# Kernel optimization log

Hardware: AMD Instinct MI355X
Metric: run time of the kernel (lower is better)

Reference implementation:

```python
import jax, jax.numpy as jnp
import numpy as np

D = 1024
W_SIZE = 512
K_ENGRAMS = 16
REPEAT = W_SIZE // K_ENGRAMS  # 32
LN_EPS = 1e-5


def setup_inputs() -> dict:
    key = jax.random.key(0)
    ks = jax.random.split(key, 6)
    B, NW = 4, 16
    engrams = jax.random.normal(ks[0], (B, NW, K_ENGRAMS, D), dtype=jnp.float32)
    pos_emb = 0.02 * jax.random.normal(ks[1], (1, 1, W_SIZE, D), dtype=jnp.float32)
    w1 = 0.02 * jax.random.normal(ks[2], (D, D), dtype=jnp.float32)
    b1 = jnp.zeros((D,), dtype=jnp.float32)
    w2 = 0.02 * jax.random.normal(ks[3], (D, D), dtype=jnp.float32)
    b2 = jnp.zeros((D,), dtype=jnp.float32)
    gamma = jnp.ones((D,), dtype=jnp.float32)
    beta = jnp.zeros((D,), dtype=jnp.float32)
    return {"engrams": engrams, "pos_emb": pos_emb, "w1": w1, "b1": b1,
            "w2": w2, "b2": b2, "gamma": gamma, "beta": beta}


def reference(engrams, pos_emb, w1, b1, w2, b2, gamma, beta):
    # (B, nw, K, d) -> (B, nw, W, d) via repeat_interleave along axis 2
    x = jnp.repeat(engrams, REPEAT, axis=2) + pos_emb
    # refine MLP: Linear -> GELU (exact) -> Linear, with residual
    h = jax.nn.gelu(jnp.einsum('bnwd,de->bnwe', x, w1.T) + b1, approximate=False)
    x = x + jnp.einsum('bnwd,de->bnwe', h, w2.T) + b2
    # LayerNorm over last dim
    mu = jnp.mean(x, axis=-1, keepdims=True)
    var = jnp.mean(jnp.square(x - mu), axis=-1, keepdims=True)
    return (x - mu) * jax.lax.rsqrt(var + LN_EPS) * gamma + beta
```

## Files before the change

### kernel.cpp

```cpp
#include <hip/hip_runtime.h>
#include <hip/hip_bf16.h>
#include <math.h>

#define D_DIM 1024
#define NROWS 32768
#define NE_ROWS 1024
#define A1_ROWS 1536
#define NT2 16

typedef __attribute__((ext_vector_type(8))) short bf16x8;
typedef __attribute__((ext_vector_type(4))) float f32x4;

static __device__ __forceinline__ ushort f2bf(float f) {
  union { float f; unsigned u; } un; un.f = f;
  unsigned u = un.u;
  unsigned r = u + 0x7fffu + ((u >> 16) & 1u);
  return (ushort)(r >> 16);
}
static __device__ __forceinline__ float bf2f(ushort h) {
  union { unsigned u; float f; } un; un.u = ((unsigned)h) << 16;
  return un.f;
}
static __device__ __forceinline__ float gelu_exact(float v) {
  return 0.5f * v * (1.0f + erff(v * 0.70710678118654752f));
}

__global__ void cast_all_kernel(const float* __restrict__ w1, const float* __restrict__ w2,
                                const float* __restrict__ eng, const float* __restrict__ pos,
                                ushort* __restrict__ dst) {
  int i = blockIdx.x * blockDim.x + threadIdx.x;
  float4 v;
  if (i < 262144) v = ((const float4*)w1)[i];
  else if (i < 524288) v = ((const float4*)w2)[i - 262144];
  else if (i < 786432) v = ((const float4*)eng)[i - 524288];
  else v = ((const float4*)pos)[i - 786432];
  ushort4 o;
  o.x = f2bf(v.x); o.y = f2bf(v.y); o.z = f2bf(v.z); o.w = f2bf(v.w);
  ((ushort4*)dst)[i] = o;
}

__global__ __launch_bounds__(256) void gemm_bt(const ushort* __restrict__ A,
                                               const ushort* __restrict__ B,
                                               float* __restrict__ C,
                                               int M, int N, int K) {
  __shared__ ushort sA[128 * 64];
  __shared__ ushort sB[128 * 64];

  int nwg = gridDim.x;
  int bid = blockIdx.x;
  if ((nwg & 7) == 0) {
    int cpx = nwg >> 3;
    bid = (bid & 7) * cpx + (bid >> 3);
  }
  int ntn = N >> 7;
  int mt = bid / ntn, nt = bid % ntn;
  int brow = mt << 7, bcol = nt << 7;

  int tid = threadIdx.x;
  int wv = tid >> 6, lane = tid & 63;
  int wm = (wv >> 1) << 6, wn = (wv & 1) << 6;
  int lr = lane & 15, lk = lane >> 4;
  int srow = lane >> 3;
  int scolsw = (((lane & 7) ^ ((lane >> 3) & 7)) << 3);

  f32x4 acc[4][4];
#pragma unroll
  for (int m = 0; m < 4; ++m)
#pragma unroll
    for (int n = 0; n < 4; ++n) acc[m][n] = (f32x4){0.f, 0.f, 0.f, 0.f};

  for (int k0 = 0; k0 < K; k0 += 64) {
    __syncthreads();
#pragma unroll
    for (int j = 0; j < 4; ++j) {
      int c = (wv << 2) + j;
      int row = (c << 3) + srow;
      const ushort* gA = A + (brow + row) * K + k0 + scolsw;
      const ushort* gB = B + (bcol + row) * K + k0 + scolsw;
      __builtin_amdgcn_global_load_lds(
          (const __attribute__((address_space(1))) unsigned int*)gA,
          (__attribute__((address_space(3))) unsigned int*)&sA[c << 9], 16, 0, 0);
      __builtin_amdgcn_global_load_lds(
          (const __attribute__((address_space(1))) unsigned int*)gB,
          (__attribute__((address_space(3))) unsigned int*)&sB[c << 9], 16, 0, 0);
    }
    __syncthreads();
#pragma unroll
    for (int kk = 0; kk < 2; ++kk) {
      int rdoff = (((kk << 2) | lk) ^ (lr & 7)) << 3;
      bf16x8 af[4], bfr[4];
#pragma unroll
      for (int m = 0; m < 4; ++m)
        af[m] = *(const bf16x8*)&sA[(wm + (m << 4) + lr) * 64 + rdoff];
#pragma unroll
      for (int n = 0; n < 4; ++n)
        bfr[n] = *(const bf16x8*)&sB[(wn + (n << 4) + lr) * 64 + rdoff];
#pragma unroll
      for (int m = 0; m < 4; ++m)
#pragma unroll
        for (int n = 0; n < 4; ++n)
          acc[m][n] = __builtin_amdgcn_mfma_f32_16x16x32_bf16(af[m], bfr[n], acc[m][n], 0, 0, 0);
    }
  }

#pragma unroll
  for (int m = 0; m < 4; ++m)
#pragma unroll
    for (int n = 0; n < 4; ++n)
#pragma unroll
      for (int i = 0; i < 4; ++i) {
        int row = brow + wm + (m << 4) + (lk << 2) + i;
        int col = bcol + wn + (n << 4) + lr;
        C[(long)row * N + col] = acc[m][n][i];
      }
}

__global__ __launch_bounds__(256) void gelu_kernel(const float* __restrict__ xw1,
                                                   const float* __restrict__ b1,
                                                   ushort* __restrict__ h) {
  int r = blockIdx.x;
  int t = threadIdx.x;
  int bn = r >> 9;
  int w = r & 511;
  int er = bn * 16 + (w >> 5);
  float4 e = ((const float4*)(xw1 + er * D_DIM))[t];
  float4 p = ((const float4*)(xw1 + (NE_ROWS + w) * D_DIM))[t];
  float4 b = ((const float4*)b1)[t];
  ushort4 o;
  o.x = f2bf(gelu_exact(e.x + p.x + b.x));
  o.y = f2bf(gelu_exact(e.y + p.y + b.y));
  o.z = f2bf(gelu_exact(e.z + p.z + b.z));
  o.w = f2bf(gelu_exact(e.w + p.w + b.w));
  ((ushort4*)(h + (long)r * D_DIM))[t] = o;
}

__global__ __launch_bounds__(512, 2) void gemm2_8ph(const ushort* __restrict__ A,
                                                    const ushort* __restrict__ B,
                                                    ushort* __restrict__ Y) {
  __shared__ ushort sA[2][2][8192];
  __shared__ ushort sB[2][2][8192];
  const int K = 1024;

  int bid = blockIdx.x;
  bid = (bid & 7) * 64 + (bid >> 3);
  int mt = bid >> 2, nt = bid & 3;
  long brow = (long)mt << 8;
  int bcol = nt << 8;

  int tid = threadIdx.x;
  int wv = tid >> 6, l = tid & 63;
  int wr = wv >> 2, wc = wv & 3;
  int lr = l & 15, lk = l >> 4;

  int sr = (wv << 4) + (l >> 2);
  int slog = ((l & 3) ^ ((l >> 3) & 3)) << 3;
  const ushort* aS = A + (brow + sr) * (long)K + slog;
  const ushort* bS = B + (size_t)(bcol + sr) * K + slog;

  int rdswz = (lk ^ ((lr >> 1) & 3)) << 3;
  int aO = (((wr << 7) + lr) << 5) + rdswz;
  int bO = (((wc << 6) + lr) << 5) + rdswz;

  f32x4 acc[8][4];
#pragma unroll
  for (int m = 0; m < 8; ++m)
#pragma unroll
    for (int n = 0; n < 4; ++n) acc[m][n] = (f32x4){0.f, 0.f, 0.f, 0.f};

#define STG(SS, SRC, kt, kkh) do {                                                   \
    int p_ = (kt) & 1; int o_ = ((kt) << 6) + ((kkh) << 5);                          \
    __builtin_amdgcn_global_load_lds(                                                \
      (const __attribute__((address_space(1))) unsigned int*)((SRC) + o_),           \
      (__attribute__((address_space(3))) unsigned int*)&SS[p_][kkh][wv << 9], 16, 0, 0); \
    __builtin_amdgcn_global_load_lds(                                                \
      (const __attribute__((address_space(1))) unsigned int*)((SRC) + o_ + 131072),  \
      (__attribute__((address_space(3))) unsigned int*)&SS[p_][kkh][(wv << 9) + 4096], 16, 0, 0); \
  } while (0)

#define BAR asm volatile("s_barrier" ::: "memory")
#define MFMA16(MOFS, BF)                                                             \
    __builtin_amdgcn_s_setprio(1);                                                   \
    _Pragma("unroll")                                                                \
    for (int m = 0; m < 4; ++m)                                                      \
      _Pragma("unroll")                                                              \
      for (int n = 0; n < 4; ++n)                                                    \
        acc[m + MOFS][n] = __builtin_amdgcn_mfma_f32_16x16x32_bf16(af[m], BF[n], acc[m + MOFS][n], 0, 0, 0); \
    __builtin_amdgcn_s_setprio(0)

  STG(sA, aS, 0, 0); STG(sB, bS, 0, 0); STG(sA, aS, 0, 1); STG(sB, bS, 0, 1);
  asm volatile("s_waitcnt vmcnt(0)" ::: "memory");
  BAR;

  for (int t = 0; t < NT2; ++t) {
    int p = t & 1;
    bf16x8 af[4], bf[4];
#pragma unroll
    for (int n = 0; n < 4; ++n) bf[n] = *(const bf16x8*)&sB[p][0][bO + (n << 9)];
#pragma unroll
    for (int m = 0; m < 4; ++m) af[m] = *(const bf16x8*)&sA[p][0][aO + (m << 9)];
    if (t + 1 < NT2) STG(sA, aS, t + 1, 0);
    BAR;
    MFMA16(0, bf);
    BAR;
#pragma unroll
    for (int m = 0; m < 4; ++m) af[m] = *(const bf16x8*)&sA[p][0][aO + ((m + 4) << 9)];
    if (t + 1 < NT2) STG(sB, bS, t + 1, 0);
    BAR;
    MFMA16(4, bf);
    if (t == NT2 - 1) asm volatile("s_waitcnt vmcnt(0)" ::: "memory");
    else              asm volatile("s_waitcnt vmcnt(4)" ::: "memory");
    BAR;
#pragma unroll
    for (int n = 0; n < 4; ++n) bf[n] = *(const bf16x8*)&sB[p][1][bO + (n << 9)];
#pragma unroll
    for (int m = 0; m < 4; ++m) af[m] = *(const bf16x8*)&sA[p][1][aO + (m << 9)];
    if (t + 1 < NT2) STG(sA, aS, t + 1, 1);
    BAR;
    MFMA16(0, bf);
    BAR;
#pragma unroll
    for (int m = 0; m < 4; ++m) af[m] = *(const bf16x8*)&sA[p][1][aO + ((m + 4) << 9)];
    if (t + 1 < NT2) STG(sB, bS, t + 1, 1);
    BAR;
    MFMA16(4, bf);
    if (t < NT2 - 1) asm volatile("s_waitcnt vmcnt(4)" ::: "memory");
    BAR;
  }
#undef STG
#undef BAR
#undef MFMA16

#pragma unroll
  for (int m = 0; m < 8; ++m)
#pragma unroll
    for (int n = 0; n < 4; ++n) {
      int col = bcol + (wc << 6) + (n << 4) + lr;
#pragma unroll
      for (int i = 0; i < 4; ++i) {
        long row = brow + (wr << 7) + (m << 4) + (lk << 2) + i;
        Y[(row << 11) + col] = f2bf(acc[m][n][i]);
      }
    }
}

__global__ __launch_bounds__(256) void ln_kernel(const float* __restrict__ eng,
                                                 const float* __restrict__ pos,
                                                 const float* __restrict__ b2,
                                                 const float* __restrict__ gamma,
                                                 const float* __restrict__ beta,
                                                 float* __restrict__ out) {
  __shared__ float red[8];
  int r = blockIdx.x;
  int t = threadIdx.x;
  int bn = r >> 9, w = r & 511;
  int er = bn * 16 + (w >> 5);
  float4 xe = ((const float4*)(eng + er * D_DIM))[t];
  float4 xp = ((const float4*)(pos + w * D_DIM))[t];
  ushort4 yv = ((const ushort4*)((const ushort*)out + ((size_t)r << 11)))[t];
  float4 bb = ((const float4*)b2)[t];
  float v0 = xe.x + xp.x + bf2f(yv.x) + bb.x;
  float v1 = xe.y + xp.y + bf2f(yv.y) + bb.y;
  float v2 = xe.z + xp.z + bf2f(yv.z) + bb.z;
  float v3 = xe.w + xp.w + bf2f(yv.w) + bb.w;
  float s  = v0 + v1 + v2 + v3;
  float sq = v0 * v0 + v1 * v1 + v2 * v2 + v3 * v3;
  int lane = t & 63, wv = t >> 6;
#pragma unroll
  for (int off = 32; off > 0; off >>= 1) {
    s  += __shfl_down(s, off);
    sq += __shfl_down(sq, off);
  }
  if (lane == 0) { red[wv] = s; red[4 + wv] = sq; }
  __syncthreads();
  float S  = red[0] + red[1] + red[2] + red[3];
  float SQ = red[4] + red[5] + red[6] + red[7];
  float mu = S * (1.0f / 1024.0f);
  float var = SQ * (1.0f / 1024.0f) - mu * mu;
  float rs = rsqrtf(var + 1e-5f);
  float4 g = ((const float4*)gamma)[t];
  float4 bt = ((const float4*)beta)[t];
  float4 o;
  o.x = (v0 - mu) * rs * g.x + bt.x;
  o.y = (v1 - mu) * rs * g.y + bt.y;
  o.z = (v2 - mu) * rs * g.z + bt.z;
  o.w = (v3 - mu) * rs * g.w + bt.w;
  ((float4*)(out + ((size_t)r << 10)))[t] = o;
}

extern "C" void kernel_launch(void* const* d_in, const int* in_sizes, int n_in,
                              void* d_out, int out_size, void* d_ws, size_t ws_size,
                              hipStream_t stream) {
  const float* eng   = (const float*)d_in[0];
  const float* pos   = (const float*)d_in[1];
  const float* w1    = (const float*)d_in[2];
  const float* b1    = (const float*)d_in[3];
  const float* w2    = (const float*)d_in[4];
  const float* b2    = (const float*)d_in[5];
  const float* gamma = (const float*)d_in[6];
  const float* beta  = (const float*)d_in[7];
  float* out = (float*)d_out;

  char* ws = (char*)d_ws;
  ushort* w1b = (ushort*)(ws);
  ushort* w2b = (ushort*)(ws + (2u << 20));
  ushort* a1b = (ushort*)(ws + (4u << 20));
  float*  xw1 = (float*)(ws + (7u << 20));
  ushort* hb  = (ushort*)(ws + (13u << 20));

  cast_all_kernel<<<3584, 256, 0, stream>>>(w1, w2, eng, pos, w1b);

  gemm_bt<<<(A1_ROWS / 128) * (D_DIM / 128), 256, 0, stream>>>(a1b, w1b, xw1,
                                                               A1_ROWS, D_DIM, D_DIM);

  gelu_kernel<<<NROWS, 256, 0, stream>>>(xw1, b1, hb);

  gemm2_8ph<<<512, 512, 0, stream>>>(hb, w2b, (ushort*)out);

  ln_kernel<<<NROWS, 256, 0, stream>>>(eng, pos, b2, gamma, beta, out);
}
```

Baseline: 173.1 us.

## Fuse GELU into second GEMM's A-tile load and fold b1 into first GEMM

```diff
diff --git a/kernel.cpp b/kernel.cpp
--- a/kernel.cpp
+++ b/kernel.cpp
@@ -20,6 +20,15 @@
 static __device__ __forceinline__ float bf2f(ushort h) {
   union { unsigned u; float f; } un; un.u = ((unsigned)h) << 16;
   return un.f;
+}
+static __device__ __forceinline__ float gelu_t(float x) {
+  float x3 = x * x * x;
+  float y = 0.7978845608f * x + 0.0356774081f * x3;
+  float ay = fabsf(y);
+  float t = __expf(-2.0f * ay);
+  float th = __fdividef(1.0f - t, 1.0f + t);
+  th = copysignf(th, y);
+  return 0.5f * x * (1.0f + th);
 }
 static __device__ __forceinline__ float gelu_exact(float v) {
   return 0.5f * v * (1.0f + erff(v * 0.70710678118654752f));
@@ -42,7 +51,9 @@
 __global__ __launch_bounds__(256) void gemm_bt(const ushort* __restrict__ A,
                                                const ushort* __restrict__ B,
                                                float* __restrict__ C,
-                                               int M, int N, int K) {
+                                               int M, int N, int K,
+                                               const float* __restrict__ bias,
+                                               int biasRow0) {
   __shared__ ushort sA[128 * 64];
   __shared__ ushort sB[128 * 64];
 
@@ -111,30 +122,13 @@
       for (int i = 0; i < 4; ++i) {
         int row = brow + wm + (m << 4) + (lk << 2) + i;
         int col = bcol + wn + (n << 4) + lr;
-        C[(long)row * N + col] = acc[m][n][i];
+        float v = acc[m][n][i];
+        if (row >= biasRow0) v += bias[col];
+        C[(long)row * N + col] = v;
       }
 }
 
-__global__ __launch_bounds__(256) void gelu_kernel(const float* __restrict__ xw1,
-                                                   const float* __restrict__ b1,
-                                                   ushort* __restrict__ h) {
-  int r = blockIdx.x;
-  int t = threadIdx.x;
-  int bn = r >> 9;
-  int w = r & 511;
-  int er = bn * 16 + (w >> 5);
-  float4 e = ((const float4*)(xw1 + er * D_DIM))[t];
-  float4 p = ((const float4*)(xw1 + (NE_ROWS + w) * D_DIM))[t];
-  float4 b = ((const float4*)b1)[t];
-  ushort4 o;
-  o.x = f2bf(gelu_exact(e.x + p.x + b.x));
-  o.y = f2bf(gelu_exact(e.y + p.y + b.y));
-  o.z = f2bf(gelu_exact(e.z + p.z + b.z));
-  o.w = f2bf(gelu_exact(e.w + p.w + b.w));
-  ((ushort4*)(h + (long)r * D_DIM))[t] = o;
-}
-
-__global__ __launch_bounds__(512, 2) void gemm2_8ph(const ushort* __restrict__ A,
+__global__ __launch_bounds__(512, 2) void gemm2_8ph(const float* __restrict__ xw1,
                                                     const ushort* __restrict__ B,
                                                     ushort* __restrict__ Y) {
   __shared__ ushort sA[2][2][8192];
@@ -146,6 +140,9 @@
   int mt = bid >> 2, nt = bid & 3;
   long brow = (long)mt << 8;
   int bcol = nt << 8;
+  int w0 = (int)(brow & 511);
+  int bn = (int)(brow >> 9);
+  int er0 = bn * 16 + (w0 >> 5);
 
   int tid = threadIdx.x;
   int wv = tid >> 6, l = tid & 63;
@@ -154,8 +151,15 @@
 
   int sr = (wv << 4) + (l >> 2);
   int slog = ((l & 3) ^ ((l >> 3) & 3)) << 3;
-  const ushort* aS = A + (brow + sr) * (long)K + slog;
   const ushort* bS = B + (size_t)(bcol + sr) * K + slog;
+
+  int ar = tid >> 1;
+  int kh = tid & 1;
+  const float* aE = xw1 + ((size_t)(er0 + (ar >> 5)) << 10) + (kh << 4);
+  const float* aP = xw1 + ((size_t)(NE_ROWS + w0 + ar) << 10) + (kh << 4);
+  int swz = (ar >> 1) & 3;
+  int wA0 = ar * 32 + ((((kh << 1) | 0) ^ swz) << 3);
+  int wA1 = ar * 32 + ((((kh << 1) | 1) ^ swz) << 3);
 
   int rdswz = (lk ^ ((lr >> 1) & 3)) << 3;
   int aO = (((wr << 7) + lr) << 5) + rdswz;
@@ -167,14 +171,37 @@
 #pragma unroll
     for (int n = 0; n < 4; ++n) acc[m][n] = (f32x4){0.f, 0.f, 0.f, 0.f};
 
-#define STG(SS, SRC, kt, kkh) do {                                                   \
+#define STGB(kt, kkh) do {                                                           \
     int p_ = (kt) & 1; int o_ = ((kt) << 6) + ((kkh) << 5);                          \
     __builtin_amdgcn_global_load_lds(                                                \
-      (const __attribute__((address_space(1))) unsigned int*)((SRC) + o_),           \
-      (__attribute__((address_space(3))) unsigned int*)&SS[p_][kkh][wv << 9], 16, 0, 0); \
+      (const __attribute__((address_space(1))) unsigned int*)(bS + o_),              \
+      (__attribute__((address_space(3))) unsigned int*)&sB[p_][kkh][wv << 9], 16, 0, 0); \
     __builtin_amdgcn_global_load_lds(                                                \
-      (const __attribute__((address_space(1))) unsigned int*)((SRC) + o_ + 131072),  \
-      (__attribute__((address_space(3))) unsigned int*)&SS[p_][kkh][(wv << 9) + 4096], 16, 0, 0); \
+      (const __attribute__((address_space(1))) unsigned int*)(bS + o_ + 131072),     \
+      (__attribute__((address_space(3))) unsigned int*)&sB[p_][kkh][(wv << 9) + 4096], 16, 0, 0); \
+  } while (0)
+
+#define LOADA(eD, pD, kb) do {                                                       \
+    _Pragma("unroll")                                                                \
+    for (int j = 0; j < 4; ++j) {                                                    \
+      eD[j] = *(const float4*)(aE + (kb) + (j << 2));                                \
+      pD[j] = *(const float4*)(aP + (kb) + (j << 2));                                \
+    }                                                                                \
+    __builtin_amdgcn_sched_barrier(0);                                               \
+  } while (0)
+
+#define WRITEA(SS, eD, pD) do {                                                      \
+    bf16x8 lo_, hi_;                                                                 \
+    lo_[0]=(short)f2bf(gelu_t(eD[0].x+pD[0].x)); lo_[1]=(short)f2bf(gelu_t(eD[0].y+pD[0].y)); \
+    lo_[2]=(short)f2bf(gelu_t(eD[0].z+pD[0].z)); lo_[3]=(short)f2bf(gelu_t(eD[0].w+pD[0].w)); \
+    lo_[4]=(short)f2bf(gelu_t(eD[1].x+pD[1].x)); lo_[5]=(short)f2bf(gelu_t(eD[1].y+pD[1].y)); \
+    lo_[6]=(short)f2bf(gelu_t(eD[1].z+pD[1].z)); lo_[7]=(short)f2bf(gelu_t(eD[1].w+pD[1].w)); \
+    hi_[0]=(short)f2bf(gelu_t(eD[2].x+pD[2].x)); hi_[1]=(short)f2bf(gelu_t(eD[2].y+pD[2].y)); \
+    hi_[2]=(short)f2bf(gelu_t(eD[2].z+pD[2].z)); hi_[3]=(short)f2bf(gelu_t(eD[2].w+pD[2].w)); \
+    hi_[4]=(short)f2bf(gelu_t(eD[3].x+pD[3].x)); hi_[5]=(short)f2bf(gelu_t(eD[3].y+pD[3].y)); \
+    hi_[6]=(short)f2bf(gelu_t(eD[3].z+pD[3].z)); hi_[7]=(short)f2bf(gelu_t(eD[3].w+pD[3].w)); \
+    *(bf16x8*)&SS[wA0] = lo_;                                                        \
+    *(bf16x8*)&SS[wA1] = hi_;                                                        \
   } while (0)
 
 #define BAR asm volatile("s_barrier" ::: "memory")
@@ -187,46 +214,58 @@
         acc[m + MOFS][n] = __builtin_amdgcn_mfma_f32_16x16x32_bf16(af[m], BF[n], acc[m + MOFS][n], 0, 0, 0); \
     __builtin_amdgcn_s_setprio(0)
 
-  STG(sA, aS, 0, 0); STG(sB, bS, 0, 0); STG(sA, aS, 0, 1); STG(sB, bS, 0, 1);
-  asm volatile("s_waitcnt vmcnt(0)" ::: "memory");
-  BAR;
+  float4 e0[4], p0[4], e1[4], p1[4];
+
+  LOADA(e0, p0, 0);
+  LOADA(e1, p1, 32);
+  WRITEA(sA[0][0], e0, p0);
+  STGB(0, 0); STGB(0, 1);
+  __syncthreads();
 
   for (int t = 0; t < NT2; ++t) {
-    int p = t & 1;
+    int p = t & 1, q = p ^ 1;
     bf16x8 af[4], bf[4];
+    if (t + 1 < NT2) LOADA(e0, p0, ((t + 1) << 6));
 #pragma unroll
     for (int n = 0; n < 4; ++n) bf[n] = *(const bf16x8*)&sB[p][0][bO + (n << 9)];
 #pragma unroll
     for (int m = 0; m < 4; ++m) af[m] = *(const bf16x8*)&sA[p][0][aO + (m << 9)];
-    if (t + 1 < NT2) STG(sA, aS, t + 1, 0);
     BAR;
     MFMA16(0, bf);
     BAR;
 #pragma unroll
     for (int m = 0; m < 4; ++m) af[m] = *(const bf16x8*)&sA[p][0][aO + ((m + 4) << 9)];
-    if (t + 1 < NT2) STG(sB, bS, t + 1, 0);
+    if (t + 1 < NT2) STGB(t + 1, 0);
     BAR;
     MFMA16(4, bf);
+    WRITEA(sA[p][1], e1, p1);
     if (t == NT2 - 1) asm volatile("s_waitcnt vmcnt(0)" ::: "memory");
-    else              asm volatile("s_waitcnt vmcnt(4)" ::: "memory");
-    BAR;
+    else              asm volatile("s_waitcnt vmcnt(10)" ::: "memory");
+    asm volatile("s_waitcnt lgkmcnt(0)" ::: "memory");
+    BAR;
+    if (t + 1 < NT2) LOADA(e1, p1, ((t + 1) << 6) + 32);
 #pragma unroll
     for (int n = 0; n < 4; ++n) bf[n] = *(const bf16x8*)&sB[p][1][bO + (n << 9)];
 #pragma unroll
     for (int m = 0; m < 4; ++m) af[m] = *(const bf16x8*)&sA[p][1][aO + (m << 9)];
-    if (t + 1 < NT2) STG(sA, aS, t + 1, 1);
     BAR;
     MFMA16(0, bf);
     BAR;
 #pragma unroll
     for (int m = 0; m < 4; ++m) af[m] = *(const bf16x8*)&sA[p][1][aO + ((m + 4) << 9)];
-    if (t + 1 < NT2) STG(sB, bS, t + 1, 1);
+    if (t + 1 < NT2) STGB(t + 1, 1);
     BAR;
     MFMA16(4, bf);
-    if (t < NT2 - 1) asm volatile("s_waitcnt vmcnt(4)" ::: "memory");
+    if (t + 1 < NT2) {
+      WRITEA(sA[q][0], e0, p0);
+      asm volatile("s_waitcnt vmcnt(10)" ::: "memory");
+    }
+    asm volatile("s_waitcnt lgkmcnt(0)" ::: "memory");
     BAR;
   }
-#undef STG
+#undef STGB
+#undef LOADA
+#undef WRITEA
 #undef BAR
 #undef MFMA16
 
@@ -305,16 +344,14 @@
   ushort* w2b = (ushort*)(ws + (2u << 20));
   ushort* a1b = (ushort*)(ws + (4u << 20));
   float*  xw1 = (float*)(ws + (7u << 20));
-  ushort* hb  = (ushort*)(ws + (13u << 20));
 
   cast_all_kernel<<<3584, 256, 0, stream>>>(w1, w2, eng, pos, w1b);
 
   gemm_bt<<<(A1_ROWS / 128) * (D_DIM / 128), 256, 0, stream>>>(a1b, w1b, xw1,
-                                                               A1_ROWS, D_DIM, D_DIM);
-
-  gelu_kernel<<<NROWS, 256, 0, stream>>>(xw1, b1, hb);
-
-  gemm2_8ph<<<512, 512, 0, stream>>>(hb, w2b, (ushort*)out);
+                                                               A1_ROWS, D_DIM, D_DIM,
+                                                               b1, NE_ROWS);
+
+  gemm2_8ph<<<512, 512, 0, stream>>>(xw1, w2b, (ushort*)out);
 
   ln_kernel<<<NROWS, 256, 0, stream>>>(eng, pos, b2, gamma, beta, out);
 }
```

Result: slower. 250.4 us (+44.7%).

## Shrink second GEMM tile to 128x128 with 256 threads and fold b1 bias

Applied to the files above, without the earlier changes.

```diff
diff --git a/kernel.cpp b/kernel.cpp
--- a/kernel.cpp
+++ b/kernel.cpp
@@ -42,7 +42,9 @@
 __global__ __launch_bounds__(256) void gemm_bt(const ushort* __restrict__ A,
                                                const ushort* __restrict__ B,
                                                float* __restrict__ C,
-                                               int M, int N, int K) {
+                                               int M, int N, int K,
+                                               const float* __restrict__ bias,
+                                               int biasRow0) {
   __shared__ ushort sA[128 * 64];
   __shared__ ushort sB[128 * 64];
 
@@ -111,12 +113,13 @@
       for (int i = 0; i < 4; ++i) {
         int row = brow + wm + (m << 4) + (lk << 2) + i;
         int col = bcol + wn + (n << 4) + lr;
-        C[(long)row * N + col] = acc[m][n][i];
+        float v = acc[m][n][i];
+        if (row >= biasRow0) v += bias[col];
+        C[(long)row * N + col] = v;
       }
 }
 
 __global__ __launch_bounds__(256) void gelu_kernel(const float* __restrict__ xw1,
-                                                   const float* __restrict__ b1,
                                                    ushort* __restrict__ h) {
   int r = blockIdx.x;
   int t = threadIdx.x;
@@ -125,119 +128,100 @@
   int er = bn * 16 + (w >> 5);
   float4 e = ((const float4*)(xw1 + er * D_DIM))[t];
   float4 p = ((const float4*)(xw1 + (NE_ROWS + w) * D_DIM))[t];
-  float4 b = ((const float4*)b1)[t];
   ushort4 o;
-  o.x = f2bf(gelu_exact(e.x + p.x + b.x));
-  o.y = f2bf(gelu_exact(e.y + p.y + b.y));
-  o.z = f2bf(gelu_exact(e.z + p.z + b.z));
-  o.w = f2bf(gelu_exact(e.w + p.w + b.w));
+  o.x = f2bf(gelu_exact(e.x + p.x));
+  o.y = f2bf(gelu_exact(e.y + p.y));
+  o.z = f2bf(gelu_exact(e.z + p.z));
+  o.w = f2bf(gelu_exact(e.w + p.w));
   ((ushort4*)(h + (long)r * D_DIM))[t] = o;
 }
 
-__global__ __launch_bounds__(512, 2) void gemm2_8ph(const ushort* __restrict__ A,
+__global__ __launch_bounds__(256, 2) void gemm2_128(const ushort* __restrict__ A,
                                                     const ushort* __restrict__ B,
                                                     ushort* __restrict__ Y) {
-  __shared__ ushort sA[2][2][8192];
-  __shared__ ushort sB[2][2][8192];
+  __shared__ ushort sA[2][2][4096];
+  __shared__ ushort sB[2][2][4096];
   const int K = 1024;
 
   int bid = blockIdx.x;
-  bid = (bid & 7) * 64 + (bid >> 3);
-  int mt = bid >> 2, nt = bid & 3;
-  long brow = (long)mt << 8;
-  int bcol = nt << 8;
+  int x = bid & 7, jj = bid >> 3;
+  int mt = (x << 5) + (jj >> 3);
+  int nt = jj & 7;
+  long brow = (long)mt << 7;
+  int bcol = nt << 7;
 
   int tid = threadIdx.x;
   int wv = tid >> 6, l = tid & 63;
-  int wr = wv >> 2, wc = wv & 3;
+  int wr = wv >> 1, wc = wv & 1;
   int lr = l & 15, lk = l >> 4;
 
-  int sr = (wv << 4) + (l >> 2);
-  int slog = ((l & 3) ^ ((l >> 3) & 3)) << 3;
-  const ushort* aS = A + (brow + sr) * (long)K + slog;
-  const ushort* bS = B + (size_t)(bcol + sr) * K + slog;
+  int srow0 = (wv << 4) + (l >> 2);
+  int slog = (((l & 3) ^ ((l >> 3) & 3)) << 3);
+  const ushort* aS = A + (brow + srow0) * (long)K + slog;
+  const ushort* bS = B + (size_t)(bcol + srow0) * K + slog;
 
   int rdswz = (lk ^ ((lr >> 1) & 3)) << 3;
-  int aO = (((wr << 7) + lr) << 5) + rdswz;
+  int aO = (((wr << 6) + lr) << 5) + rdswz;
   int bO = (((wc << 6) + lr) << 5) + rdswz;
 
-  f32x4 acc[8][4];
-#pragma unroll
-  for (int m = 0; m < 8; ++m)
+  f32x4 acc[4][4];
+#pragma unroll
+  for (int m = 0; m < 4; ++m)
 #pragma unroll
     for (int n = 0; n < 4; ++n) acc[m][n] = (f32x4){0.f, 0.f, 0.f, 0.f};
 
-#define STG(SS, SRC, kt, kkh) do {                                                   \
-    int p_ = (kt) & 1; int o_ = ((kt) << 6) + ((kkh) << 5);                          \
-    __builtin_amdgcn_global_load_lds(                                                \
-      (const __attribute__((address_space(1))) unsigned int*)((SRC) + o_),           \
-      (__attribute__((address_space(3))) unsigned int*)&SS[p_][kkh][wv << 9], 16, 0, 0); \
-    __builtin_amdgcn_global_load_lds(                                                \
-      (const __attribute__((address_space(1))) unsigned int*)((SRC) + o_ + 131072),  \
-      (__attribute__((address_space(3))) unsigned int*)&SS[p_][kkh][(wv << 9) + 4096], 16, 0, 0); \
-  } while (0)
+#define STG(kt, kkh) do {                                                            \
+    int p_ = (kt) & 1; int ko_ = ((kt) << 6) + ((kkh) << 5);                         \
+    _Pragma("unroll")                                                                \
+    for (int j2 = 0; j2 < 2; ++j2) {                                                 \
+      __builtin_amdgcn_global_load_lds(                                              \
+        (const __attribute__((address_space(1))) unsigned int*)(aS + ko_ + (long)(j2 << 6) * K), \
+        (__attribute__((address_space(3))) unsigned int*)&sA[p_][kkh][(j2 << 11) + (wv << 9)], 16, 0, 0); \
+      __builtin_amdgcn_global_load_lds(                                              \
+        (const __attribute__((address_space(1))) unsigned int*)(bS + ko_ + (long)(j2 << 6) * K), \
+        (__attribute__((address_space(3))) unsigned int*)&sB[p_][kkh][(j2 << 11) + (wv << 9)], 16, 0, 0); \
+    } } while (0)
 
 #define BAR asm volatile("s_barrier" ::: "memory")
-#define MFMA16(MOFS, BF)                                                             \
-    __builtin_amdgcn_s_setprio(1);                                                   \
-    _Pragma("unroll")                                                                \
-    for (int m = 0; m < 4; ++m)                                                      \
-      _Pragma("unroll")                                                              \
-      for (int n = 0; n < 4; ++n)                                                    \
-        acc[m + MOFS][n] = __builtin_amdgcn_mfma_f32_16x16x32_bf16(af[m], BF[n], acc[m + MOFS][n], 0, 0, 0); \
-    __builtin_amdgcn_s_setprio(0)
-
-  STG(sA, aS, 0, 0); STG(sB, bS, 0, 0); STG(sA, aS, 0, 1); STG(sB, bS, 0, 1);
-  asm volatile("s_waitcnt vmcnt(0)" ::: "memory");
+
+  STG(0, 0); STG(0, 1);
+  asm volatile("s_waitcnt vmcnt(4)" ::: "memory");
   BAR;
 
   for (int t = 0; t < NT2; ++t) {
     int p = t & 1;
-    bf16x8 af[4], bf[4];
-#pragma unroll
-    for (int n = 0; n < 4; ++n) bf[n] = *(const bf16x8*)&sB[p][0][bO + (n << 9)];
-#pragma unroll
-    for (int m = 0; m < 4; ++m) af[m] = *(const bf16x8*)&sA[p][0][aO + (m << 9)];
-    if (t + 1 < NT2) STG(sA, aS, t + 1, 0);
-    BAR;
-    MFMA16(0, bf);
-    BAR;
-#pragma unroll
-    for (int m = 0; m < 4; ++m) af[m] = *(const bf16x8*)&sA[p][0][aO + ((m + 4) << 9)];
-    if (t + 1 < NT2) STG(sB, bS, t + 1, 0);
-    BAR;
-    MFMA16(4, bf);
-    if (t == NT2 - 1) asm volatile("s_waitcnt vmcnt(0)" ::: "memory");
-    else              asm volatile("s_waitcnt vmcnt(4)" ::: "memory");
-    BAR;
-#pragma unroll
-    for (int n = 0; n < 4; ++n) bf[n] = *(const bf16x8*)&sB[p][1][bO + (n << 9)];
-#pragma unroll
-    for (int m = 0; m < 4; ++m) af[m] = *(const bf16x8*)&sA[p][1][aO + (m << 9)];
-    if (t + 1 < NT2) STG(sA, aS, t + 1, 1);
-    BAR;
-    MFMA16(0, bf);
-    BAR;
-#pragma unroll
-    for (int m = 0; m < 4; ++m) af[m] = *(const bf16x8*)&sA[p][1][aO + ((m + 4) << 9)];
-    if (t + 1 < NT2) STG(sB, bS, t + 1, 1);
-    BAR;
-    MFMA16(4, bf);
-    if (t < NT2 - 1) asm volatile("s_waitcnt vmcnt(4)" ::: "memory");
-    BAR;
+#pragma unroll
+    for (int kk = 0; kk < 2; ++kk) {
+      bf16x8 af[4], bf[4];
+#pragma unroll
+      for (int n = 0; n < 4; ++n) bf[n] = *(const bf16x8*)&sB[p][kk][bO + (n << 9)];
+#pragma unroll
+      for (int m = 0; m < 4; ++m) af[m] = *(const bf16x8*)&sA[p][kk][aO + (m << 9)];
+      if (t + 1 < NT2) STG(t + 1, kk);
+      BAR;
+      __builtin_amdgcn_s_setprio(1);
+#pragma unroll
+      for (int m = 0; m < 4; ++m)
+#pragma unroll
+        for (int n = 0; n < 4; ++n)
+          acc[m][n] = __builtin_amdgcn_mfma_f32_16x16x32_bf16(af[m], bf[n], acc[m][n], 0, 0, 0);
+      __builtin_amdgcn_s_setprio(0);
+      if (t + 1 < NT2) asm volatile("s_waitcnt vmcnt(4)" ::: "memory");
+      else             asm volatile("s_waitcnt vmcnt(0)" ::: "memory");
+      BAR;
+    }
   }
 #undef STG
 #undef BAR
-#undef MFMA16
-
-#pragma unroll
-  for (int m = 0; m < 8; ++m)
+
+#pragma unroll
+  for (int m = 0; m < 4; ++m)
 #pragma unroll
     for (int n = 0; n < 4; ++n) {
       int col = bcol + (wc << 6) + (n << 4) + lr;
 #pragma unroll
       for (int i = 0; i < 4; ++i) {
-        long row = brow + (wr << 7) + (m << 4) + (lk << 2) + i;
+        long row = brow + (wr << 6) + (m << 4) + (lk << 2) + i;
         Y[(row << 11) + col] = f2bf(acc[m][n][i]);
       }
     }
@@ -310,11 +294,12 @@
   cast_all_kernel<<<3584, 256, 0, stream>>>(w1, w2, eng, pos, w1b);
 
   gemm_bt<<<(A1_ROWS / 128) * (D_DIM / 128), 256, 0, stream>>>(a1b, w1b, xw1,
-                                                               A1_ROWS, D_DIM, D_DIM);
-
-  gelu_kernel<<<NROWS, 256, 0, stream>>>(xw1, b1, hb);
-
-  gemm2_8ph<<<512, 512, 0, stream>>>(hb, w2b, (ushort*)out);
+                                                               A1_ROWS, D_DIM, D_DIM,
+                                                               b1, NE_ROWS);
+
+  gelu_kernel<<<NROWS, 256, 0, stream>>>(xw1, hb);
+
+  gemm2_128<<<2048, 256, 0, stream>>>(hb, w2b, (ushort*)out);
 
   ln_kernel<<<NROWS, 256, 0, stream>>>(eng, pos, b2, gamma, beta, out);
 }
```

After: 178.9 us. 1.03x slower.
